# Kernel optimization log

Measured on AMD Instinct MI355X. Metric: run time of the kernel, lower is better.

The kernel has to match this reference:

```python
import jax, jax.numpy as jnp
import numpy as np

DK = 128  # key/query head dim (also value dim)

def setup_inputs() -> dict:
    key = jax.random.key(0)
    k1, k2, k3, k4 = jax.random.split(key, 4)
    query = jax.random.normal(k1, (8, 512, 28, 28), dtype=jnp.float32)
    support = jax.random.normal(k2, (16, 512, 28, 28), dtype=jnp.float32)
    Wk = jax.random.normal(k3, (128, 512), dtype=jnp.float32) * (1.0 / np.sqrt(512.0))
    Wv = jax.random.normal(k4, (128, 512), dtype=jnp.float32) * (1.0 / np.sqrt(512.0))
    return {"query": query, "support": support, "Wk": Wk, "Wv": Wv}

def reference(query, support, Wk, Wv):
    B, D, H, W = query.shape
    N, Ds, Hs, Ws = support.shape
    q_flat = query.reshape(B, D, H * W)        # b d u
    s_flat = support.reshape(N, Ds, Hs * Ws)   # n d v
    # 1x1 convs == channel projections (query_head is aliased to key_head)
    q = jnp.einsum('kd,bdu->bku', Wk, q_flat)            # B dk u
    query_value = jnp.einsum('kd,bdu->bku', Wv, q_flat)  # B dv u
    support_key = jnp.einsum('kd,ndv->nkv', Wk, s_flat)  # N dk v
    support_value = jnp.einsum('kd,ndv->nkv', Wv, s_flat)  # N dv v
    scores = jnp.einsum('bku,nkv->bnuv', q, support_key) / jnp.sqrt(jnp.float32(DK))
    # first softmax over dim=3 in the source is dead code (overwritten); effective
    # attention is softmax over the support-class axis n (dim=1)
    attn = jax.nn.softmax(scores, axis=1)  # B N u v
    # note: u is summed out here, exactly as in the source einsum
    query_aligned = jnp.einsum('bnuv,nkv->bkv', attn, support_value)  # B dv v
    a = query_aligned.transpose(0, 2, 1)   # B v dv
    b = query_value.transpose(0, 2, 1)     # B u dv
    # cdist(p=2)**2 == squared euclidean distances; compute without forming diffs
    a2 = jnp.sum(a * a, axis=-1)  # B v
    b2 = jnp.sum(b * b, axis=-1)  # B u
    ab = jnp.einsum('bpd,brd->bpr', a, b)  # B v u
    d2 = jnp.maximum(a2[:, :, None] + b2[:, None, :] - 2.0 * ab, 0.0)
    P, R = d2.shape[1], d2.shape[2]
    return jnp.sum(d2, axis=(1, 2)) / (P * R)  # (B,)
```

## Files before the change

### kernel.cpp

```cpp
#include <hip/hip_runtime.h>

#define U_CNT 784
#define DKH   128
#define DD    512
#define NQ    8
#define NS    16

typedef short bf16x8 __attribute__((ext_vector_type(8)));
typedef float f32x4  __attribute__((ext_vector_type(4)));

__device__ __forceinline__ unsigned short f2bf(float f) {
  unsigned u = __builtin_bit_cast(unsigned, f);
  u += 0x7fffu + ((u >> 16) & 1u);
  return (unsigned short)(u >> 16);
}


__global__ void cast_w(const float* __restrict__ Wk, const float* __restrict__ Wv,
                       unsigned short* __restrict__ Wkv_f) {
  int i = blockIdx.x * 256 + threadIdx.x;
  int f = i >> 6, l = i & 63;
  int r = f >> 4, ds = f & 15;
  int col = l & 15, rowg = l >> 4;
  int ko = r * 16 + col;
  int d0 = ds * 32 + rowg * 8;
  const float* src = (ko < 128) ? (Wk + (size_t)ko * 512 + d0)
                                : (Wv + (size_t)(ko - 128) * 512 + d0);
  unsigned short o[8];
#pragma unroll
  for (int j = 0; j < 8; ++j) o[j] = f2bf(src[j]);
  ushort4 lo = {o[0], o[1], o[2], o[3]}, hi = {o[4], o[5], o[6], o[7]};
  *(ushort4*)(Wkv_f + (size_t)i * 8) = lo;
  *(ushort4*)(Wkv_f + (size_t)i * 8 + 4) = hi;
}

__global__ __launch_bounds__(256)
void xpose_kernel(const float* __restrict__ query, const float* __restrict__ support,
                  unsigned short* __restrict__ x_f) {
  __shared__ unsigned short lds[784 * 34];
  int s = blockIdx.x;
  int m = blockIdx.y;
  const float* X = (m < 8) ? (query + (size_t)m * DD * U_CNT)
                           : (support + (size_t)(m - 8) * DD * U_CNT);
  int tid = threadIdx.x;
  for (int i = 0; i < 25; ++i) {
    int idx = i * 256 + tid;
    if (idx < 6272) {
      int row = idx / 196, c4 = idx - row * 196;
      float4 v = *(const float4*)(X + (size_t)(s * 32 + row) * U_CNT + c4 * 4);
      float vv[4] = {v.x, v.y, v.z, v.w};
#pragma unroll
      for (int cc = 0; cc < 4; ++cc) {
        int p = c4 * 4 + cc;
        int sw = row ^ ((p & 15) << 1);
        lds[p * 34 + sw] = f2bf(vv[cc]);
      }
    }
  }
  __syncthreads();
  unsigned short* xb = x_f + (size_t)m * 401408;
  for (int i = 0; i < 49; ++i) {
    int idx = i * 256 + tid;
    int pt = idx >> 8, rem = idx & 255;
    int cl = rem >> 6, q2 = rem & 63, ul = q2 >> 2, jj = (q2 & 3) * 2;
    int p = pt * 16 + ul;
    int dl = cl * 8 + jj;
    int sw = dl ^ ((p & 15) << 1);
    ushort2 o = *(const ushort2*)(&lds[p * 34 + sw]);
    *(ushort2*)(xb + (size_t)pt * 8192 + (s * 4 + cl) * 128 + ul * 8 + jj) = o;
  }
}

__global__ __launch_bounds__(256, 4)
void proj_kernel(const unsigned short* __restrict__ x_f,
                 const unsigned short* __restrict__ Wkv_f,
                 unsigned short* __restrict__ q_f, unsigned short* __restrict__ sk_f,
                 float* __restrict__ sv_t, float* __restrict__ S1p, float* __restrict__ S2p) {
  int pt = blockIdx.x;
  int m  = blockIdx.y;
  int tid = threadIdx.x;
  int wave = tid >> 6, l = tid & 63;
  int col = l & 15, rowg = l >> 4;

  const unsigned short* xb =
      x_f + (size_t)m * 401408 + (size_t)pt * 8192 + l * 8;
  const unsigned short* wb = Wkv_f + (size_t)(wave * 4) * 16 * 512 + l * 8;
  f32x4 acc[4];
  f32x4 zero = {0.f, 0.f, 0.f, 0.f};
#pragma unroll
  for (int rr = 0; rr < 4; ++rr) acc[rr] = zero;

  bf16x8 Bcur = *(const bf16x8*)(xb);
  for (int ds = 0; ds < 16; ++ds) {
    int nds = (ds + 1 < 16) ? ds + 1 : ds;
    bf16x8 Bnxt = *(const bf16x8*)(xb + nds * 512);
    bf16x8 Af[4];
#pragma unroll
    for (int rr = 0; rr < 4; ++rr)
      Af[rr] = *(const bf16x8*)(wb + (size_t)(rr * 16 + ds) * 512);
#pragma unroll
    for (int rr = 0; rr < 4; ++rr)
      acc[rr] = __builtin_amdgcn_mfma_f32_16x16x32_bf16(Af[rr], Bcur, acc[rr], 0, 0, 0);
    Bcur = Bnxt;
  }

  if (m < 8) {
    if (wave < 2) {
#pragma unroll
      for (int rr = 0; rr < 4; ++rr) {
        int r = wave * 4 + rr;
        const float sc = 0.12751744f;
        ushort4 o;
        o.x = f2bf(acc[rr][0] * sc); o.y = f2bf(acc[rr][1] * sc);
        o.z = f2bf(acc[rr][2] * sc); o.w = f2bf(acc[rr][3] * sc);
        size_t off = (size_t)m * 100352 + (size_t)pt * 2048 +
                     (size_t)(2 * r + (rowg >> 1)) * 128 + col * 8 + (rowg & 1) * 4;
        *(ushort4*)(q_f + off) = o;
      }
    } else {
      float s1 = 0.f;
#pragma unroll
      for (int rr = 0; rr < 4; ++rr) {
        int r = wave * 4 + rr;
#pragma unroll
        for (int j = 0; j < 4; ++j) {
          float x = acc[rr][j];
          s1 += x * x;
          x += __shfl_xor(x, 1, 64); x += __shfl_xor(x, 2, 64);
          x += __shfl_xor(x, 4, 64); x += __shfl_xor(x, 8, 64);
          if (col == 0)
            S2p[((size_t)pt * 8 + m) * DKH + (r - 8) * 16 + rowg * 4 + j] = x;
        }
      }
#pragma unroll
      for (int o = 32; o >= 1; o >>= 1) s1 += __shfl_xor(s1, o, 64);
      if (l == 0) S1p[((wave - 2) * 49 + pt) * 8 + m] = s1;
    }
  } else {
    int img = m - 8;
    if (wave < 2) {
#pragma unroll
      for (int rr = 0; rr < 4; ++rr) {
        int r = wave * 4 + rr;
        ushort4 o;
        o.x = f2bf(acc[rr][0]); o.y = f2bf(acc[rr][1]);
        o.z = f2bf(acc[rr][2]); o.w = f2bf(acc[rr][3]);
        size_t off = (size_t)(pt * 16 + col) * 2048 +
                     (size_t)(2 * r + (rowg >> 1)) * 128 + img * 8 + (rowg & 1) * 4;
        *(ushort4*)(sk_f + off) = o;
      }
    } else {
#pragma unroll
      for (int rr = 0; rr < 4; ++rr) {
        int r = wave * 4 + rr;
        int kb = (r - 8) * 16 + rowg * 4;
        float4 o = make_float4(acc[rr][0], acc[rr][1], acc[rr][2], acc[rr][3]);
        *(float4*)(sv_t + (size_t)(img * U_CNT + pt * 16 + col) * DKH + kb) = o;
      }
    }
  }
}

__global__ __launch_bounds__(256, 4)
void score_kernel(const unsigned short* __restrict__ q_f,
                  const unsigned short* __restrict__ sk_f,
                  float* __restrict__ w_part) {
  int bx = blockIdx.x;
  int vb = bx % 49;
  int uc = (bx / 49) & 3;
  int b  = bx / 196;
  int wv = threadIdx.x >> 6;
  int l  = threadIdx.x & 63;
  int col = l & 15, rowg = l >> 4;
  int vbase = vb * 16 + wv * 4;

  bf16x8 A[4][4];
#pragma unroll
  for (int v = 0; v < 4; ++v) {
    const unsigned short* ap = sk_f + (size_t)(vbase + v) * 2048 + rowg * 128 + col * 8;
#pragma unroll
    for (int s = 0; s < 4; ++s) A[v][s] = *(const bf16x8*)(ap + s * 512);
  }

  float wl[4][4];
#pragma unroll
  for (int v = 0; v < 4; ++v)
#pragma unroll
    for (int j = 0; j < 4; ++j) wl[v][j] = 0.f;

  int ut0 = (uc == 0) ? 0 : uc * 12 + 1;
  int cnt = (uc == 0) ? 13 : 12;
  const unsigned short* qb = q_f + (size_t)b * 100352 + rowg * 128 + col * 8;
  f32x4 zero = {0.f, 0.f, 0.f, 0.f};

  const unsigned short* qp0 = qb + (size_t)ut0 * 2048;
  bf16x8 B0 = *(const bf16x8*)(qp0);
  bf16x8 B1 = *(const bf16x8*)(qp0 + 512);
  bf16x8 B2 = *(const bf16x8*)(qp0 + 1024);
  bf16x8 B3 = *(const bf16x8*)(qp0 + 1536);

  for (int it = 0; it < cnt; ++it) {
    int nit = (it + 1 < cnt) ? it + 1 : it;
    const unsigned short* qp = qb + (size_t)(ut0 + nit) * 2048;
    bf16x8 N0 = *(const bf16x8*)(qp);
    bf16x8 N1 = *(const bf16x8*)(qp + 512);
    bf16x8 N2 = *(const bf16x8*)(qp + 1024);
    bf16x8 N3 = *(const bf16x8*)(qp + 1536);

    f32x4 acc[4];
#pragma unroll
    for (int v = 0; v < 4; ++v) acc[v] = zero;
#pragma unroll
    for (int v = 0; v < 4; ++v)
      acc[v] = __builtin_amdgcn_mfma_f32_16x16x32_bf16(A[v][0], B0, acc[v], 0, 0, 0);
#pragma unroll
    for (int v = 0; v < 4; ++v)
      acc[v] = __builtin_amdgcn_mfma_f32_16x16x32_bf16(A[v][1], B1, acc[v], 0, 0, 0);
#pragma unroll
    for (int v = 0; v < 4; ++v)
      acc[v] = __builtin_amdgcn_mfma_f32_16x16x32_bf16(A[v][2], B2, acc[v], 0, 0, 0);
#pragma unroll
    for (int v = 0; v < 4; ++v)
      acc[v] = __builtin_amdgcn_mfma_f32_16x16x32_bf16(A[v][3], B3, acc[v], 0, 0, 0);
#pragma unroll
    for (int v = 0; v < 4; ++v) {
      float e0 = __builtin_amdgcn_exp2f(acc[v][0]);
      float e1 = __builtin_amdgcn_exp2f(acc[v][1]);
      float e2 = __builtin_amdgcn_exp2f(acc[v][2]);
      float e3 = __builtin_amdgcn_exp2f(acc[v][3]);
      float ps = (e0 + e1) + (e2 + e3);
      ps += __shfl_xor(ps, 16, 64);
      ps += __shfl_xor(ps, 32, 64);
      float r = __builtin_amdgcn_rcpf(ps);
      wl[v][0] += e0 * r; wl[v][1] += e1 * r;
      wl[v][2] += e2 * r; wl[v][3] += e3 * r;
    }
    B0 = N0; B1 = N1; B2 = N2; B3 = N3;
  }
#pragma unroll
  for (int v = 0; v < 4; ++v)
#pragma unroll
    for (int j = 0; j < 4; ++j) {
      float x = wl[v][j];
      x += __shfl_xor(x, 1, 64); x += __shfl_xor(x, 2, 64);
      x += __shfl_xor(x, 4, 64); x += __shfl_xor(x, 8, 64);
      wl[v][j] = x;
    }
  __shared__ float wst[4][4][16];
#pragma unroll
  for (int v = 0; v < 4; ++v)
    if (col == v) {
#pragma unroll
      for (int j = 0; j < 4; ++j) wst[wv][v][rowg * 4 + j] = wl[v][j];
    }
  __syncthreads();
  int t = threadIdx.x;
  int vl = t >> 4, c = t & 15;
  w_part[(((size_t)uc * 8 + b) * U_CNT + vb * 16 + vl) * NS + c] =
      wst[vl >> 2][vl & 3][c];
}

__global__ __launch_bounds__(256)
void align_kernel(const float* __restrict__ w_part, const float* __restrict__ sv_t,
                  float* __restrict__ T1p, float* __restrict__ T2p) {
  int vt2 = blockIdx.x;
  int t = threadIdx.x;
  __shared__ float w_sh[2][8][16];
  {
    int vl = t >> 7, b = (t >> 4) & 7, n = t & 15;
    float s = 0.f;
#pragma unroll
    for (int uc = 0; uc < 4; ++uc)
      s += w_part[(((size_t)uc * 8 + b) * U_CNT + vt2 * 2 + vl) * NS + n];
    w_sh[vl][b][n] = s;
  }
  __syncthreads();
  int k = t & 127, vl = t >> 7;
  int v = vt2 * 2 + vl;
  float a[8];
#pragma unroll
  for (int b = 0; b < 8; ++b) a[b] = 0.f;
#pragma unroll
  for (int n = 0; n < NS; ++n) {
    float s = sv_t[((size_t)n * U_CNT + v) * DKH + k];
#pragma unroll
    for (int b = 0; b < 8; ++b) a[b] += w_sh[vl][b][n] * s;
  }
  __shared__ float red[8][128];
  if (vl == 1) {
#pragma unroll
    for (int b = 0; b < 8; ++b) red[b][k] = a[b];
  }
  __syncthreads();
  if (vl == 0) {
#pragma unroll
    for (int b = 0; b < 8; ++b)
      T2p[((size_t)vt2 * 8 + b) * DKH + k] = a[b] + red[b][k];
  }
  __shared__ float sw1[4][8];
#pragma unroll
  for (int b = 0; b < 8; ++b) {
    float x = a[b] * a[b];
#pragma unroll
    for (int o = 32; o >= 1; o >>= 1) x += __shfl_xor(x, o, 64);
    if ((t & 63) == 0) sw1[t >> 6][b] = x;
  }
  __syncthreads();
  if (t < 8) T1p[vt2 * 8 + t] = sw1[0][t] + sw1[1][t] + sw1[2][t] + sw1[3][t];
}

__global__ __launch_bounds__(256)
void reduce_partials(const float* __restrict__ S1p, const float* __restrict__ T1p,
                     const float* __restrict__ S2p, const float* __restrict__ T2p,
                     float* __restrict__ S2, float* __restrict__ T2,
                     float* __restrict__ ST1) {
  __shared__ float smem[264];
  int bx = blockIdx.x, t = threadIdx.x;
  if (bx < 32) {
    int b = bx >> 2, kq = bx & 3;
    int kl = t & 31, g = t >> 5;
    int k = kq * 32 + kl;
    float s = 0.f;
    for (int w = g; w < 392; w += 8)
      s += T2p[((size_t)w * 8 + b) * DKH + k];
    smem[g * 32 + kl] = s;
    __syncthreads();
    if (t < 32) {
      float v = 0.f;
#pragma unroll
      for (int g2 = 0; g2 < 8; ++g2) v += smem[g2 * 32 + t];
      T2[b * DKH + kq * 32 + t] = v;
    }
  } else {
    int b = bx - 32;
    int k = t & 127, h = t >> 7;
    float s = 0.f;
    for (int w = h; w < 49; w += 2)
      s += S2p[((size_t)w * 8 + b) * DKH + k];
    if (h == 1) smem[k] = s;
    __syncthreads();
    if (h == 0) S2[b * DKH + k] = s + smem[k];
    float c = 0.f;
    for (int i = t; i < 98; i += 256)  c += S1p[i * 8 + b];
    for (int i = t; i < 392; i += 256) c += T1p[i * 8 + b];
#pragma unroll
    for (int o = 32; o >= 1; o >>= 1) c += __shfl_xor(c, o, 64);
    if ((t & 63) == 0) smem[256 + (t >> 6)] = c;
    __syncthreads();
    if (t == 0) ST1[b] = smem[256] + smem[257] + smem[258] + smem[259];
  }
}

__global__ void final_kernel(const float* __restrict__ S2, const float* __restrict__ T2,
                             const float* __restrict__ ST1, float* __restrict__ out) {
  int b = blockIdx.x, t = threadIdx.x;
  float p = S2[b * DKH + t] * T2[b * DKH + t];
#pragma unroll
  for (int o = 32; o >= 1; o >>= 1) p += __shfl_xor(p, o, 64);
  __shared__ float s2[2];
  if ((t & 63) == 0) s2[t >> 6] = p;
  __syncthreads();
  if (t == 0)
    out[b] = (784.0f * ST1[b] - 2.0f * (s2[0] + s2[1])) * (1.0f / (784.0f * 784.0f));
}

extern "C" void kernel_launch(void* const* d_in, const int* in_sizes, int n_in,
                              void* d_out, int out_size, void* d_ws, size_t ws_size,
                              hipStream_t stream) {
  const float* query   = (const float*)d_in[0];
  const float* support = (const float*)d_in[1];
  const float* Wk      = (const float*)d_in[2];
  const float* Wv      = (const float*)d_in[3];
  float* out = (float*)d_out;
  char* ws = (char*)d_ws;

  unsigned short* Wkv_f = (unsigned short*)(ws + 0);
  unsigned short* q_f  = (unsigned short*)(ws + 262144);
  unsigned short* sk_f = (unsigned short*)(ws + 1867776);
  float*          sv_t = (float*)(ws + 5079040);
  float*          w_part = (float*)(ws + 11501568);
  unsigned short* x_f  = (unsigned short*)(ws + 13107200);
  float*          S1p  = (float*)(ws + 32374784);
  float*          T1p  = (float*)(ws + 32378880);
  float*          S2p  = (float*)(ws + 32395264);
  float*          T2p  = (float*)(ws + 32595968);
  float*          S2   = (float*)(ws + 34201600);
  float*          T2   = (float*)(ws + 34205696);
  float*          ST1  = (float*)(ws + 34209792);
  if (ws_size < (size_t)34210000) return;

  cast_w<<<64, 256, 0, stream>>>(Wk, Wv, Wkv_f);
  xpose_kernel<<<dim3(16, 24), 256, 0, stream>>>(query, support, x_f);
  proj_kernel<<<dim3(49, 24), 256, 0, stream>>>(x_f, Wkv_f, q_f, sk_f, sv_t, S1p, S2p);
  score_kernel<<<1568, 256, 0, stream>>>(q_f, sk_f, w_part);
  align_kernel<<<392, 256, 0, stream>>>(w_part, sv_t, T1p, T2p);
  reduce_partials<<<40, 256, 0, stream>>>(S1p, T1p, S2p, T2p, S2, T2, ST1);
  final_kernel<<<8, 128, 0, stream>>>(S2, T2, ST1, out);
}
```

Before: 162.4 us.

## Merge prep kernels, widen transpose stores, double proj tiles, fuse final reductions

The weight cast and the input transpose now run in one launch. The transpose uses a new LDS swizzle with 16-byte reads and writes instead of 4-byte ones. The projection kernel handles two position tiles per block so each weight fragment load feeds twice as many MFMAs. The partial-reduction and final kernels are merged into a single 8-block kernel. Together these remove two launches and cut memory instruction count, at the cost of more registers in proj and less parallelism in the final reduction.

New measurement: 196.2 us. +20.8%, slower.

```diff
diff --git a/kernel.cpp b/kernel.cpp
--- a/kernel.cpp
+++ b/kernel.cpp
@@ -3,7 +3,6 @@
 #define U_CNT 784
 #define DKH   128
 #define DD    512
-#define NQ    8
 #define NS    16
 
 typedef short bf16x8 __attribute__((ext_vector_type(8)));
@@ -16,33 +15,32 @@
 }
 
 
-__global__ void cast_w(const float* __restrict__ Wk, const float* __restrict__ Wv,
-                       unsigned short* __restrict__ Wkv_f) {
-  int i = blockIdx.x * 256 + threadIdx.x;
-  int f = i >> 6, l = i & 63;
-  int r = f >> 4, ds = f & 15;
-  int col = l & 15, rowg = l >> 4;
-  int ko = r * 16 + col;
-  int d0 = ds * 32 + rowg * 8;
-  const float* src = (ko < 128) ? (Wk + (size_t)ko * 512 + d0)
-                                : (Wv + (size_t)(ko - 128) * 512 + d0);
-  unsigned short o[8];
-#pragma unroll
-  for (int j = 0; j < 8; ++j) o[j] = f2bf(src[j]);
-  ushort4 lo = {o[0], o[1], o[2], o[3]}, hi = {o[4], o[5], o[6], o[7]};
-  *(ushort4*)(Wkv_f + (size_t)i * 8) = lo;
-  *(ushort4*)(Wkv_f + (size_t)i * 8 + 4) = hi;
-}
-
 __global__ __launch_bounds__(256)
-void xpose_kernel(const float* __restrict__ query, const float* __restrict__ support,
-                  unsigned short* __restrict__ x_f) {
-  __shared__ unsigned short lds[784 * 34];
-  int s = blockIdx.x;
-  int m = blockIdx.y;
+void prep_kernel(const float* __restrict__ query, const float* __restrict__ support,
+                 const float* __restrict__ Wk, const float* __restrict__ Wv,
+                 unsigned short* __restrict__ x_f, unsigned short* __restrict__ Wkv_f) {
+  int bx = blockIdx.x, tid = threadIdx.x;
+  if (bx >= 384) {
+    int i = (bx - 384) * 256 + tid;
+    int f = i >> 6, l = i & 63;
+    int r = f >> 4, ds = f & 15;
+    int col = l & 15, rowg = l >> 4;
+    int ko = r * 16 + col;
+    int d0 = ds * 32 + rowg * 8;
+    const float* src = (ko < 128) ? (Wk + (size_t)ko * 512 + d0)
+                                  : (Wv + (size_t)(ko - 128) * 512 + d0);
+    unsigned short o[8];
+#pragma unroll
+    for (int j = 0; j < 8; ++j) o[j] = f2bf(src[j]);
+    ushort4 lo = {o[0], o[1], o[2], o[3]}, hi = {o[4], o[5], o[6], o[7]};
+    *(ushort4*)(Wkv_f + (size_t)i * 8) = lo;
+    *(ushort4*)(Wkv_f + (size_t)i * 8 + 4) = hi;
+    return;
+  }
+  __shared__ unsigned short lds[784 * 40];
+  int s = bx & 15, m = bx >> 4;
   const float* X = (m < 8) ? (query + (size_t)m * DD * U_CNT)
                            : (support + (size_t)(m - 8) * DD * U_CNT);
-  int tid = threadIdx.x;
   for (int i = 0; i < 25; ++i) {
     int idx = i * 256 + tid;
     if (idx < 6272) {
@@ -52,22 +50,30 @@
 #pragma unroll
       for (int cc = 0; cc < 4; ++cc) {
         int p = c4 * 4 + cc;
-        int sw = row ^ ((p & 15) << 1);
-        lds[p * 34 + sw] = f2bf(vv[cc]);
+        int q = (p & 15) ^ ((p >> 5) & 3);
+        lds[p * 40 + (row ^ (q << 1))] = f2bf(vv[cc]);
       }
     }
   }
   __syncthreads();
   unsigned short* xb = x_f + (size_t)m * 401408;
-  for (int i = 0; i < 49; ++i) {
+  for (int i = 0; i < 13; ++i) {
     int idx = i * 256 + tid;
-    int pt = idx >> 8, rem = idx & 255;
-    int cl = rem >> 6, q2 = rem & 63, ul = q2 >> 2, jj = (q2 & 3) * 2;
-    int p = pt * 16 + ul;
-    int dl = cl * 8 + jj;
-    int sw = dl ^ ((p & 15) << 1);
-    ushort2 o = *(const ushort2*)(&lds[p * 34 + sw]);
-    *(ushort2*)(xb + (size_t)pt * 8192 + (s * 4 + cl) * 128 + ul * 8 + jj) = o;
+    if (idx < 3136) {
+      int pt = idx >> 6, rem = idx & 63;
+      int cl = rem >> 4, ul = rem & 15;
+      int p = pt * 16 + ul;
+      int q = (p & 15) ^ ((p >> 5) & 3);
+      int4 D = *(const int4*)(&lds[p * 40 + 8 * (cl ^ ((q >> 2) & 3))]);
+      int sel = q & 3;
+      int d0 = D.x, d1 = D.y, d2 = D.z, d3 = D.w;
+      int a0 = (sel & 1) ? d1 : d0, a1 = (sel & 1) ? d0 : d1;
+      int a2 = (sel & 1) ? d3 : d2, a3 = (sel & 1) ? d2 : d3;
+      int4 O;
+      O.x = (sel & 2) ? a2 : a0; O.y = (sel & 2) ? a3 : a1;
+      O.z = (sel & 2) ? a0 : a2; O.w = (sel & 2) ? a1 : a3;
+      *(int4*)(xb + (size_t)pt * 8192 + (s * 4 + cl) * 128 + ul * 8) = O;
+    }
   }
 }
 
@@ -76,86 +82,98 @@
                  const unsigned short* __restrict__ Wkv_f,
                  unsigned short* __restrict__ q_f, unsigned short* __restrict__ sk_f,
                  float* __restrict__ sv_t, float* __restrict__ S1p, float* __restrict__ S2p) {
-  int pt = blockIdx.x;
+  int pt0 = blockIdx.x * 2;
   int m  = blockIdx.y;
   int tid = threadIdx.x;
   int wave = tid >> 6, l = tid & 63;
   int col = l & 15, rowg = l >> 4;
-
-  const unsigned short* xb =
-      x_f + (size_t)m * 401408 + (size_t)pt * 8192 + l * 8;
+  int npt = (pt0 + 1 < 49) ? 2 : 1;
+  int pt1 = (npt == 2) ? pt0 + 1 : pt0;
+
+  const unsigned short* xb0 = x_f + (size_t)m * 401408 + (size_t)pt0 * 8192 + l * 8;
+  const unsigned short* xb1 = x_f + (size_t)m * 401408 + (size_t)pt1 * 8192 + l * 8;
   const unsigned short* wb = Wkv_f + (size_t)(wave * 4) * 16 * 512 + l * 8;
-  f32x4 acc[4];
+  f32x4 acc[2][4];
   f32x4 zero = {0.f, 0.f, 0.f, 0.f};
 #pragma unroll
-  for (int rr = 0; rr < 4; ++rr) acc[rr] = zero;
-
-  bf16x8 Bcur = *(const bf16x8*)(xb);
+  for (int pi = 0; pi < 2; ++pi)
+#pragma unroll
+    for (int rr = 0; rr < 4; ++rr) acc[pi][rr] = zero;
+
+  bf16x8 B0c = *(const bf16x8*)(xb0);
+  bf16x8 B1c = *(const bf16x8*)(xb1);
   for (int ds = 0; ds < 16; ++ds) {
     int nds = (ds + 1 < 16) ? ds + 1 : ds;
-    bf16x8 Bnxt = *(const bf16x8*)(xb + nds * 512);
+    bf16x8 B0n = *(const bf16x8*)(xb0 + nds * 512);
+    bf16x8 B1n = *(const bf16x8*)(xb1 + nds * 512);
     bf16x8 Af[4];
 #pragma unroll
     for (int rr = 0; rr < 4; ++rr)
       Af[rr] = *(const bf16x8*)(wb + (size_t)(rr * 16 + ds) * 512);
 #pragma unroll
     for (int rr = 0; rr < 4; ++rr)
-      acc[rr] = __builtin_amdgcn_mfma_f32_16x16x32_bf16(Af[rr], Bcur, acc[rr], 0, 0, 0);
-    Bcur = Bnxt;
-  }
-
-  if (m < 8) {
-    if (wave < 2) {
-#pragma unroll
-      for (int rr = 0; rr < 4; ++rr) {
-        int r = wave * 4 + rr;
-        const float sc = 0.12751744f;
-        ushort4 o;
-        o.x = f2bf(acc[rr][0] * sc); o.y = f2bf(acc[rr][1] * sc);
-        o.z = f2bf(acc[rr][2] * sc); o.w = f2bf(acc[rr][3] * sc);
-        size_t off = (size_t)m * 100352 + (size_t)pt * 2048 +
-                     (size_t)(2 * r + (rowg >> 1)) * 128 + col * 8 + (rowg & 1) * 4;
-        *(ushort4*)(q_f + off) = o;
+      acc[0][rr] = __builtin_amdgcn_mfma_f32_16x16x32_bf16(Af[rr], B0c, acc[0][rr], 0, 0, 0);
+#pragma unroll
+    for (int rr = 0; rr < 4; ++rr)
+      acc[1][rr] = __builtin_amdgcn_mfma_f32_16x16x32_bf16(Af[rr], B1c, acc[1][rr], 0, 0, 0);
+    B0c = B0n; B1c = B1n;
+  }
+
+  for (int pi = 0; pi < npt; ++pi) {
+    int pt = pt0 + pi;
+    if (m < 8) {
+      if (wave < 2) {
+#pragma unroll
+        for (int rr = 0; rr < 4; ++rr) {
+          int r = wave * 4 + rr;
+          const float sc = 0.12751744f;
+          ushort4 o;
+          o.x = f2bf(acc[pi][rr][0] * sc); o.y = f2bf(acc[pi][rr][1] * sc);
+          o.z = f2bf(acc[pi][rr][2] * sc); o.w = f2bf(acc[pi][rr][3] * sc);
+          size_t off = (size_t)m * 100352 + (size_t)pt * 2048 +
+                       (size_t)(2 * r + (rowg >> 1)) * 128 + col * 8 + (rowg & 1) * 4;
+          *(ushort4*)(q_f + off) = o;
+        }
+      } else {
+        float s1 = 0.f;
+#pragma unroll
+        for (int rr = 0; rr < 4; ++rr) {
+          int r = wave * 4 + rr;
+#pragma unroll
+          for (int j = 0; j < 4; ++j) {
+            float x = acc[pi][rr][j];
+            s1 += x * x;
+            x += __shfl_xor(x, 1, 64); x += __shfl_xor(x, 2, 64);
+            x += __shfl_xor(x, 4, 64); x += __shfl_xor(x, 8, 64);
+            if (col == 0)
+              S2p[((size_t)pt * 8 + m) * DKH + (r - 8) * 16 + rowg * 4 + j] = x;
+          }
+        }
+#pragma unroll
+        for (int o = 32; o >= 1; o >>= 1) s1 += __shfl_xor(s1, o, 64);
+        if (l == 0) S1p[((wave - 2) * 49 + pt) * 8 + m] = s1;
       }
     } else {
-      float s1 = 0.f;
-#pragma unroll
-      for (int rr = 0; rr < 4; ++rr) {
-        int r = wave * 4 + rr;
-#pragma unroll
-        for (int j = 0; j < 4; ++j) {
-          float x = acc[rr][j];
-          s1 += x * x;
-          x += __shfl_xor(x, 1, 64); x += __shfl_xor(x, 2, 64);
-          x += __shfl_xor(x, 4, 64); x += __shfl_xor(x, 8, 64);
-          if (col == 0)
-            S2p[((size_t)pt * 8 + m) * DKH + (r - 8) * 16 + rowg * 4 + j] = x;
+      int img = m - 8;
+      if (wave < 2) {
+#pragma unroll
+        for (int rr = 0; rr < 4; ++rr) {
+          int r = wave * 4 + rr;
+          ushort4 o;
+          o.x = f2bf(acc[pi][rr][0]); o.y = f2bf(acc[pi][rr][1]);
+          o.z = f2bf(acc[pi][rr][2]); o.w = f2bf(acc[pi][rr][3]);
+          size_t off = (size_t)(pt * 16 + col) * 2048 +
+                       (size_t)(2 * r + (rowg >> 1)) * 128 + img * 8 + (rowg & 1) * 4;
+          *(ushort4*)(sk_f + off) = o;
         }
-      }
-#pragma unroll
-      for (int o = 32; o >= 1; o >>= 1) s1 += __shfl_xor(s1, o, 64);
-      if (l == 0) S1p[((wave - 2) * 49 + pt) * 8 + m] = s1;
-    }
-  } else {
-    int img = m - 8;
-    if (wave < 2) {
-#pragma unroll
-      for (int rr = 0; rr < 4; ++rr) {
-        int r = wave * 4 + rr;
-        ushort4 o;
-        o.x = f2bf(acc[rr][0]); o.y = f2bf(acc[rr][1]);
-        o.z = f2bf(acc[rr][2]); o.w = f2bf(acc[rr][3]);
-        size_t off = (size_t)(pt * 16 + col) * 2048 +
-                     (size_t)(2 * r + (rowg >> 1)) * 128 + img * 8 + (rowg & 1) * 4;
-        *(ushort4*)(sk_f + off) = o;
-      }
-    } else {
-#pragma unroll
-      for (int rr = 0; rr < 4; ++rr) {
-        int r = wave * 4 + rr;
-        int kb = (r - 8) * 16 + rowg * 4;
-        float4 o = make_float4(acc[rr][0], acc[rr][1], acc[rr][2], acc[rr][3]);
-        *(float4*)(sv_t + (size_t)(img * U_CNT + pt * 16 + col) * DKH + kb) = o;
+      } else {
+#pragma unroll
+        for (int rr = 0; rr < 4; ++rr) {
+          int r = wave * 4 + rr;
+          int kb = (r - 8) * 16 + rowg * 4;
+          float4 o = make_float4(acc[pi][rr][0], acc[pi][rr][1], acc[pi][rr][2], acc[pi][rr][3]);
+          *(float4*)(sv_t + (size_t)(img * U_CNT + pt * 16 + col) * DKH + kb) = o;
+        }
       }
     }
   }
@@ -310,58 +328,30 @@
 }
 
 __global__ __launch_bounds__(256)
-void reduce_partials(const float* __restrict__ S1p, const float* __restrict__ T1p,
-                     const float* __restrict__ S2p, const float* __restrict__ T2p,
-                     float* __restrict__ S2, float* __restrict__ T2,
-                     float* __restrict__ ST1) {
-  __shared__ float smem[264];
-  int bx = blockIdx.x, t = threadIdx.x;
-  if (bx < 32) {
-    int b = bx >> 2, kq = bx & 3;
-    int kl = t & 31, g = t >> 5;
-    int k = kq * 32 + kl;
-    float s = 0.f;
-    for (int w = g; w < 392; w += 8)
-      s += T2p[((size_t)w * 8 + b) * DKH + k];
-    smem[g * 32 + kl] = s;
-    __syncthreads();
-    if (t < 32) {
-      float v = 0.f;
-#pragma unroll
-      for (int g2 = 0; g2 < 8; ++g2) v += smem[g2 * 32 + t];
-      T2[b * DKH + kq * 32 + t] = v;
-    }
-  } else {
-    int b = bx - 32;
-    int k = t & 127, h = t >> 7;
-    float s = 0.f;
-    for (int w = h; w < 49; w += 2)
-      s += S2p[((size_t)w * 8 + b) * DKH + k];
-    if (h == 1) smem[k] = s;
-    __syncthreads();
-    if (h == 0) S2[b * DKH + k] = s + smem[k];
-    float c = 0.f;
-    for (int i = t; i < 98; i += 256)  c += S1p[i * 8 + b];
-    for (int i = t; i < 392; i += 256) c += T1p[i * 8 + b];
-#pragma unroll
-    for (int o = 32; o >= 1; o >>= 1) c += __shfl_xor(c, o, 64);
-    if ((t & 63) == 0) smem[256 + (t >> 6)] = c;
-    __syncthreads();
-    if (t == 0) ST1[b] = smem[256] + smem[257] + smem[258] + smem[259];
-  }
-}
-
-__global__ void final_kernel(const float* __restrict__ S2, const float* __restrict__ T2,
-                             const float* __restrict__ ST1, float* __restrict__ out) {
+void final_kernel(const float* __restrict__ S1p, const float* __restrict__ T1p,
+                  const float* __restrict__ S2p, const float* __restrict__ T2p,
+                  float* __restrict__ out) {
   int b = blockIdx.x, t = threadIdx.x;
-  float p = S2[b * DKH + t] * T2[b * DKH + t];
-#pragma unroll
-  for (int o = 32; o >= 1; o >>= 1) p += __shfl_xor(p, o, 64);
-  __shared__ float s2[2];
-  if ((t & 63) == 0) s2[t >> 6] = p;
+  int k = t & 127, h = t >> 7;
+  float s2s = 0.f, t2s = 0.f;
+  for (int w = h; w < 49; w += 2)  s2s += S2p[((size_t)w * 8 + b) * DKH + k];
+  for (int w = h; w < 392; w += 2) t2s += T2p[((size_t)w * 8 + b) * DKH + k];
+  float c = 0.f;
+  for (int i = t; i < 98; i += 256)  c += S1p[i * 8 + b];
+  for (int i = t; i < 392; i += 256) c += T1p[i * 8 + b];
+  __shared__ float c2[2][128];
+  if (h == 1) { c2[0][k] = s2s; c2[1][k] = t2s; }
+  __syncthreads();
+  float prod = 0.f;
+  if (h == 0) prod = (s2s + c2[0][k]) * (t2s + c2[1][k]);
+  float val = 784.0f * c - 2.0f * prod;
+#pragma unroll
+  for (int o = 32; o >= 1; o >>= 1) val += __shfl_xor(val, o, 64);
+  __shared__ float sw[4];
+  if ((t & 63) == 0) sw[t >> 6] = val;
   __syncthreads();
   if (t == 0)
-    out[b] = (784.0f * ST1[b] - 2.0f * (s2[0] + s2[1])) * (1.0f / (784.0f * 784.0f));
+    out[b] = (sw[0] + sw[1] + sw[2] + sw[3]) * (1.0f / (784.0f * 784.0f));
 }
 
 extern "C" void kernel_launch(void* const* d_in, const int* in_sizes, int n_in,
@@ -384,16 +374,11 @@
   float*          T1p  = (float*)(ws + 32378880);
   float*          S2p  = (float*)(ws + 32395264);
   float*          T2p  = (float*)(ws + 32595968);
-  float*          S2   = (float*)(ws + 34201600);
-  float*          T2   = (float*)(ws + 34205696);
-  float*          ST1  = (float*)(ws + 34209792);
   if (ws_size < (size_t)34210000) return;
 
-  cast_w<<<64, 256, 0, stream>>>(Wk, Wv, Wkv_f);
-  xpose_kernel<<<dim3(16, 24), 256, 0, stream>>>(query, support, x_f);
-  proj_kernel<<<dim3(49, 24), 256, 0, stream>>>(x_f, Wkv_f, q_f, sk_f, sv_t, S1p, S2p);
+  prep_kernel<<<448, 256, 0, stream>>>(query, support, Wk, Wv, x_f, Wkv_f);
+  proj_kernel<<<dim3(25, 24), 256, 0, stream>>>(x_f, Wkv_f, q_f, sk_f, sv_t, S1p, S2p);
   score_kernel<<<1568, 256, 0, stream>>>(q_f, sk_f, w_part);
   align_kernel<<<392, 256, 0, stream>>>(w_part, sv_t, T1p, T2p);
-  reduce_partials<<<40, 256, 0, stream>>>(S1p, T1p, S2p, T2p, S2, T2, ST1);
-  final_kernel<<<8, 128, 0, stream>>>(S2, T2, ST1, out);
-}
+  final_kernel<<<8, 256, 0, stream>>>(S1p, T1p, S2p, T2p, out);
+}
```
